# Kernel optimization log

Hardware: AMD Instinct MI355X
Metric: run time of the kernel (lower is better)

Reference implementation:

```python
import jax, jax.numpy as jnp
import numpy as np

NEG_INF = -jnp.inf


def _bilinear_resize(x, out_h, out_w):
    """Matches torch F.interpolate(mode='bilinear', align_corners=False, antialias=False).
    x: [N, C, H, W] -> [N, C, out_h, out_w]."""
    N, C, H, W = x.shape

    def idx(in_s, out_s):
        scale = in_s / out_s
        src = jnp.maximum((jnp.arange(out_s, dtype=jnp.float32) + 0.5) * scale - 0.5, 0.0)
        i0 = jnp.floor(src).astype(jnp.int32)
        i1 = jnp.minimum(i0 + 1, in_s - 1)
        w = src - i0.astype(jnp.float32)
        return i0, i1, w

    y0, y1, wy = idx(H, out_h)
    x0, x1, wx = idx(W, out_w)
    # blend rows
    top = x[:, :, y0, :] * (1.0 - wy)[None, None, :, None] + x[:, :, y1, :] * wy[None, None, :, None]
    # blend cols
    out = top[:, :, :, x0] * (1.0 - wx)[None, None, None, :] + top[:, :, :, x1] * wx[None, None, None, :]
    return out


def _maxpool2(x):
    return jax.lax.reduce_window(x, NEG_INF, jax.lax.max,
                                 (1, 1, 2, 2), (1, 1, 2, 2), 'VALID')


def _lrelu(x):
    return jnp.where(x >= 0, x, 0.2 * x)


def setup_inputs() -> dict:
    key = jax.random.key(0)
    ks = jax.random.split(key, 6)
    N, C, H, W = 4, 32, 256, 256
    KS2 = 9
    psf = jax.random.normal(ks[0], (N, C, H, W), dtype=jnp.float32)
    featuremap = jax.random.normal(ks[1], (N, C, H, W), dtype=jnp.float32)
    w1 = jax.random.normal(ks[2], (C * KS2, C), dtype=jnp.float32) * 0.05
    b1 = jnp.zeros((C * KS2,), dtype=jnp.float32)
    ws = jax.random.normal(ks[3], (C * KS2, C), dtype=jnp.float32) * 0.05
    bs = jnp.zeros((C * KS2,), dtype=jnp.float32)
    return {"psf": psf, "featuremap": featuremap, "w1": w1, "b1": b1, "ws": ws, "bs": bs}


def reference(psf, featuremap, w1, b1, ws, bs):
    N, C, H, W = featuremap.shape
    KS = 3
    # psf branch: 1/4 bilinear -> maxpool2 -> KPResBlock (1x1 convs) -> x8 bilinear
    p = _bilinear_resize(psf, H // 4, W // 4)
    p = _maxpool2(p)                       # [N, C, H/8, W/8]
    identity = jnp.einsum('nchw,oc->nohw', p, ws) + bs[None, :, None, None]
    y = _lrelu(jnp.einsum('nchw,oc->nohw', p, w1) + b1[None, :, None, None]) + identity
    filt = _bilinear_resize(y, H, W)       # [N, C*9, H, W]
    # FAC: per-pixel dynamic 3x3 filter, fused (no materialized unfold)
    wflt = filt.reshape(N, C, KS * KS, H, W)
    padded = jnp.pad(featuremap, ((0, 0), (0, 0), (1, 1), (1, 1)))
    out = jnp.zeros((N, C, H, W), dtype=featuremap.dtype)
    for dy in range(KS):
        for dx in range(KS):
            out = out + padded[:, :, dy:dy + H, dx:dx + W] * wflt[:, :, dy * KS + dx]
    return out
```

## Files before the change

### kernel.cpp

```cpp
#include <hip/hip_runtime.h>

#define N_ 4
#define C_ 32
#define H_ 256
#define W_ 256
#define O_ 288
#define PH 32
#define P_ELEMS (N_*C_*PH*PH)
#define Y_ELEMS (N_*O_*PH*PH)
#define OUT_ELEMS (N_*C_*H_*W_)

__global__ __launch_bounds__(256) void k_downsample(
    const float* __restrict__ psf, float* __restrict__ p) {
  int tid = blockIdx.x * blockDim.x + threadIdx.x;
  if (tid >= P_ELEMS) return;
  int tx = tid & 31;
  int ty = (tid >> 5) & 31;
  int nc = tid >> 10;
  const float* x = psf + (size_t)nc * (H_ * W_);
  float m = -1e30f;
#pragma unroll
  for (int a = 0; a < 2; a++) {
#pragma unroll
    for (int b = 0; b < 2; b++) {
      int r0 = 8 * ty + 4 * a + 1;
      int c0 = 8 * tx + 4 * b + 1;
      const float* row0 = x + r0 * W_ + c0;
      const float* row1 = row0 + W_;
      float avg = 0.25f * (row0[0] + row0[1] + row1[0] + row1[1]);
      m = fmaxf(m, avg);
    }
  }
  p[tid] = m;
}

__global__ __launch_bounds__(256) void k_conv1x1(
    const float* __restrict__ p, const float* __restrict__ w1,
    const float* __restrict__ b1, const float* __restrict__ ws,
    const float* __restrict__ bs, float* __restrict__ y) {
  int bid = blockIdx.x;
  int n = bid / O_;
  int o = bid - n * O_;
  const float4* p4 = (const float4*)(p + (size_t)n * (C_ * PH * PH));
  const float* w1o = w1 + o * C_;
  const float* wso = ws + o * C_;
  float bb1 = b1[o];
  float bbs = bs[o];
  int t = threadIdx.x;
  float a1x = bb1, a1y = bb1, a1z = bb1, a1w = bb1;
  float a2x = bbs, a2y = bbs, a2z = bbs, a2w = bbs;
#pragma unroll
  for (int c = 0; c < C_; c++) {
    float4 pv = p4[c * 256 + t];
    float u1 = w1o[c], u2 = wso[c];
    a1x = fmaf(pv.x, u1, a1x); a1y = fmaf(pv.y, u1, a1y);
    a1z = fmaf(pv.z, u1, a1z); a1w = fmaf(pv.w, u1, a1w);
    a2x = fmaf(pv.x, u2, a2x); a2y = fmaf(pv.y, u2, a2y);
    a2z = fmaf(pv.z, u2, a2z); a2w = fmaf(pv.w, u2, a2w);
  }
  float4 r;
  r.x = ((a1x >= 0.f) ? a1x : 0.2f * a1x) + a2x;
  r.y = ((a1y >= 0.f) ? a1y : 0.2f * a1y) + a2y;
  r.z = ((a1z >= 0.f) ? a1z : 0.2f * a1z) + a2z;
  r.w = ((a1w >= 0.f) ? a1w : 0.2f * a1w) + a2w;
  ((float4*)(y + (size_t)bid * (PH * PH)))[t] = r;
}

__global__ __launch_bounds__(256) void k_fac(
    const float* __restrict__ fm, const float* __restrict__ y,
    float* __restrict__ out) {
  int bid = blockIdx.x;
  int work = (bid >> 3) + (bid & 7) * 512;
  int g = (work << 8) + threadIdx.x;
  int m = g & 31;
  int h = (g >> 5) & 255;
  int c = (g >> 13) & 31;
  int n = g >> 18;

  float sh = fmaxf(0.125f * (float)h - 0.4375f, 0.f);
  int y0 = (int)sh;
  float wy = sh - (float)y0;
  int y1 = min(y0 + 1, 31);

  int cm1 = max(m - 1, 0);
  int cp1 = min(m + 1, 31);
  int ro0 = y0 * 32, ro1 = y1 * 32;

  const float* yb = y + ((size_t)(n * O_ + c * 9) << 10);
  const float* fb = fm + ((size_t)(n * C_ + c) << 16);

  float acc0 = 0.f, acc1 = 0.f, acc2 = 0.f, acc3 = 0.f;
  float acc4 = 0.f, acc5 = 0.f, acc6 = 0.f, acc7 = 0.f;

#pragma unroll
  for (int ky = 0; ky < 3; ky++) {
    int row = h + ky - 1;
    float fv[10];
    if (row >= 0 && row < 256) {
      const float* fr = fb + row * 256 + (m << 3);
      float4 q0 = *(const float4*)(fr);
      float4 q1 = *(const float4*)(fr + 4);
      fv[0] = (m > 0) ? fr[-1] : 0.f;
      fv[1] = q0.x; fv[2] = q0.y; fv[3] = q0.z; fv[4] = q0.w;
      fv[5] = q1.x; fv[6] = q1.y; fv[7] = q1.z; fv[8] = q1.w;
      fv[9] = (m < 31) ? fr[8] : 0.f;
    } else {
#pragma unroll
      for (int t = 0; t < 10; t++) fv[t] = 0.f;
    }
#pragma unroll
    for (int kx = 0; kx < 3; kx++) {
      const float* yp = yb + ((3 * ky + kx) << 10);
      float t0 = yp[ro0 + cm1], t1 = yp[ro0 + m], t2 = yp[ro0 + cp1];
      float u0 = yp[ro1 + cm1], u1 = yp[ro1 + m], u2 = yp[ro1 + cp1];
      float tb0 = fmaf(wy, u0 - t0, t0);
      float tb1 = fmaf(wy, u1 - t1, t1);
      float tb2 = fmaf(wy, u2 - t2, t2);
      float d0 = tb1 - tb0;
      float d1 = tb2 - tb1;
      float yv0 = fmaf(0.5625f, d0, tb0);
      float yv1 = fmaf(0.6875f, d0, tb0);
      float yv2 = fmaf(0.8125f, d0, tb0);
      float yv3 = fmaf(0.9375f, d0, tb0);
      float yv4 = fmaf(0.0625f, d1, tb1);
      float yv5 = fmaf(0.1875f, d1, tb1);
      float yv6 = fmaf(0.3125f, d1, tb1);
      float yv7 = fmaf(0.4375f, d1, tb1);
      acc0 = fmaf(fv[0 + kx], yv0, acc0);
      acc1 = fmaf(fv[1 + kx], yv1, acc1);
      acc2 = fmaf(fv[2 + kx], yv2, acc2);
      acc3 = fmaf(fv[3 + kx], yv3, acc3);
      acc4 = fmaf(fv[4 + kx], yv4, acc4);
      acc5 = fmaf(fv[5 + kx], yv5, acc5);
      acc6 = fmaf(fv[6 + kx], yv6, acc6);
      acc7 = fmaf(fv[7 + kx], yv7, acc7);
    }
  }
  float* ob = out + ((size_t)(((n * C_ + c) << 8) + h) << 8) + (m << 3);
  float4 r0 = {acc0, acc1, acc2, acc3};
  float4 r1 = {acc4, acc5, acc6, acc7};
  *(float4*)(ob) = r0;
  *(float4*)(ob + 4) = r1;
}

extern "C" void kernel_launch(void* const* d_in, const int* in_sizes, int n_in,
                              void* d_out, int out_size, void* d_ws,
                              size_t ws_size, hipStream_t stream) {
  const float* psf = (const float*)d_in[0];
  const float* fm = (const float*)d_in[1];
  const float* w1 = (const float*)d_in[2];
  const float* b1 = (const float*)d_in[3];
  const float* ws = (const float*)d_in[4];
  const float* bs = (const float*)d_in[5];
  float* out = (float*)d_out;

  float* p = (float*)d_ws;
  float* y = p + P_ELEMS;

  k_downsample<<<P_ELEMS / 256, 256, 0, stream>>>(psf, p);
  k_conv1x1<<<N_ * O_, 256, 0, stream>>>(p, w1, b1, ws, bs, y);
  k_fac<<<OUT_ELEMS / (8 * 256), 256, 0, stream>>>(fm, y, out);
}
```

Before: 131.8 us.

## Interleave 9 filter taps per position in y and use nontemporal output stores

The conv1x1 kernel now computes all 9 taps for one channel per thread and writes them contiguously with a stride of 12 floats per spatial position. The FAC kernel can then gather the 6 neighbouring positions with vector loads and precompute the row blend once for all taps, replacing 54 scattered scalar loads with 12 vector loads plus 6 scalars. Output stores become nontemporal so they bypass cache pollution. The y buffer grows by the padding factor, and the conv kernel now runs fewer blocks, each with more registers.

```diff
diff --git a/kernel.cpp b/kernel.cpp
--- a/kernel.cpp
+++ b/kernel.cpp
@@ -4,11 +4,12 @@
 #define C_ 32
 #define H_ 256
 #define W_ 256
-#define O_ 288
 #define PH 32
+#define KSTRIDE 12
 #define P_ELEMS (N_*C_*PH*PH)
-#define Y_ELEMS (N_*O_*PH*PH)
 #define OUT_ELEMS (N_*C_*H_*W_)
+
+typedef float v4f __attribute__((ext_vector_type(4)));
 
 __global__ __launch_bounds__(256) void k_downsample(
     const float* __restrict__ psf, float* __restrict__ p) {
@@ -39,31 +40,36 @@
     const float* __restrict__ b1, const float* __restrict__ ws,
     const float* __restrict__ bs, float* __restrict__ y) {
   int bid = blockIdx.x;
-  int n = bid / O_;
-  int o = bid - n * O_;
-  const float4* p4 = (const float4*)(p + (size_t)n * (C_ * PH * PH));
-  const float* w1o = w1 + o * C_;
-  const float* wso = ws + o * C_;
-  float bb1 = b1[o];
-  float bbs = bs[o];
-  int t = threadIdx.x;
-  float a1x = bb1, a1y = bb1, a1z = bb1, a1w = bb1;
-  float a2x = bbs, a2y = bbs, a2z = bbs, a2w = bbs;
+  int q = bid & 3;
+  int c = (bid >> 2) & 31;
+  int n = bid >> 7;
+  int hw = (q << 8) + threadIdx.x;
+  const float* pn = p + ((n * C_) << 10) + hw;
+  float a1[9], a2[9];
 #pragma unroll
-  for (int c = 0; c < C_; c++) {
-    float4 pv = p4[c * 256 + t];
-    float u1 = w1o[c], u2 = wso[c];
-    a1x = fmaf(pv.x, u1, a1x); a1y = fmaf(pv.y, u1, a1y);
-    a1z = fmaf(pv.z, u1, a1z); a1w = fmaf(pv.w, u1, a1w);
-    a2x = fmaf(pv.x, u2, a2x); a2y = fmaf(pv.y, u2, a2y);
-    a2z = fmaf(pv.z, u2, a2z); a2w = fmaf(pv.w, u2, a2w);
+  for (int k = 0; k < 9; k++) {
+    a1[k] = b1[c * 9 + k];
+    a2[k] = bs[c * 9 + k];
   }
-  float4 r;
-  r.x = ((a1x >= 0.f) ? a1x : 0.2f * a1x) + a2x;
-  r.y = ((a1y >= 0.f) ? a1y : 0.2f * a1y) + a2y;
-  r.z = ((a1z >= 0.f) ? a1z : 0.2f * a1z) + a2z;
-  r.w = ((a1w >= 0.f) ? a1w : 0.2f * a1w) + a2w;
-  ((float4*)(y + (size_t)bid * (PH * PH)))[t] = r;
+#pragma unroll
+  for (int c2 = 0; c2 < C_; c2++) {
+    float pv = pn[c2 << 10];
+#pragma unroll
+    for (int k = 0; k < 9; k++) {
+      a1[k] = fmaf(pv, w1[(c * 9 + k) * C_ + c2], a1[k]);
+      a2[k] = fmaf(pv, ws[(c * 9 + k) * C_ + c2], a2[k]);
+    }
+  }
+  float r[9];
+#pragma unroll
+  for (int k = 0; k < 9; k++)
+    r[k] = ((a1[k] >= 0.f) ? a1[k] : 0.2f * a1[k]) + a2[k];
+  float* yo = y + (size_t)(((n * C_ + c) << 10) + hw) * KSTRIDE;
+  v4f v0 = {r[0], r[1], r[2], r[3]};
+  v4f v1 = {r[4], r[5], r[6], r[7]};
+  *(v4f*)yo = v0;
+  *(v4f*)(yo + 4) = v1;
+  yo[8] = r[8];
 }
 
 __global__ __launch_bounds__(256) void k_fac(
@@ -81,14 +87,31 @@
   int y0 = (int)sh;
   float wy = sh - (float)y0;
   int y1 = min(y0 + 1, 31);
-
   int cm1 = max(m - 1, 0);
   int cp1 = min(m + 1, 31);
-  int ro0 = y0 * 32, ro1 = y1 * 32;
 
-  const float* yb = y + ((size_t)(n * O_ + c * 9) << 10);
+  const float* yb = y + (size_t)((n * C_ + c) << 10) * KSTRIDE;
+  int pos[6] = {(y0 << 5) + cm1, (y0 << 5) + m, (y0 << 5) + cp1,
+                (y1 << 5) + cm1, (y1 << 5) + m, (y1 << 5) + cp1};
+  float P[6][9];
+#pragma unroll
+  for (int i = 0; i < 6; i++) {
+    const float* qp = yb + pos[i] * KSTRIDE;
+    v4f A = *(const v4f*)qp;
+    v4f B = *(const v4f*)(qp + 4);
+    P[i][0] = A.x; P[i][1] = A.y; P[i][2] = A.z; P[i][3] = A.w;
+    P[i][4] = B.x; P[i][5] = B.y; P[i][6] = B.z; P[i][7] = B.w;
+    P[i][8] = qp[8];
+  }
+  float TB0[9], TB1[9], TB2[9];
+#pragma unroll
+  for (int k = 0; k < 9; k++) {
+    TB0[k] = fmaf(wy, P[3][k] - P[0][k], P[0][k]);
+    TB1[k] = fmaf(wy, P[4][k] - P[1][k], P[1][k]);
+    TB2[k] = fmaf(wy, P[5][k] - P[2][k], P[2][k]);
+  }
+
   const float* fb = fm + ((size_t)(n * C_ + c) << 16);
-
   float acc0 = 0.f, acc1 = 0.f, acc2 = 0.f, acc3 = 0.f;
   float acc4 = 0.f, acc5 = 0.f, acc6 = 0.f, acc7 = 0.f;
 
@@ -97,9 +120,9 @@
     int row = h + ky - 1;
     float fv[10];
     if (row >= 0 && row < 256) {
-      const float* fr = fb + row * 256 + (m << 3);
-      float4 q0 = *(const float4*)(fr);
-      float4 q1 = *(const float4*)(fr + 4);
+      const float* fr = fb + (row << 8) + (m << 3);
+      v4f q0 = *(const v4f*)(fr);
+      v4f q1 = *(const v4f*)(fr + 4);
       fv[0] = (m > 0) ? fr[-1] : 0.f;
       fv[1] = q0.x; fv[2] = q0.y; fv[3] = q0.z; fv[4] = q0.w;
       fv[5] = q1.x; fv[6] = q1.y; fv[7] = q1.z; fv[8] = q1.w;
@@ -110,37 +133,24 @@
     }
 #pragma unroll
     for (int kx = 0; kx < 3; kx++) {
-      const float* yp = yb + ((3 * ky + kx) << 10);
-      float t0 = yp[ro0 + cm1], t1 = yp[ro0 + m], t2 = yp[ro0 + cp1];
-      float u0 = yp[ro1 + cm1], u1 = yp[ro1 + m], u2 = yp[ro1 + cp1];
-      float tb0 = fmaf(wy, u0 - t0, t0);
-      float tb1 = fmaf(wy, u1 - t1, t1);
-      float tb2 = fmaf(wy, u2 - t2, t2);
-      float d0 = tb1 - tb0;
-      float d1 = tb2 - tb1;
-      float yv0 = fmaf(0.5625f, d0, tb0);
-      float yv1 = fmaf(0.6875f, d0, tb0);
-      float yv2 = fmaf(0.8125f, d0, tb0);
-      float yv3 = fmaf(0.9375f, d0, tb0);
-      float yv4 = fmaf(0.0625f, d1, tb1);
-      float yv5 = fmaf(0.1875f, d1, tb1);
-      float yv6 = fmaf(0.3125f, d1, tb1);
-      float yv7 = fmaf(0.4375f, d1, tb1);
-      acc0 = fmaf(fv[0 + kx], yv0, acc0);
-      acc1 = fmaf(fv[1 + kx], yv1, acc1);
-      acc2 = fmaf(fv[2 + kx], yv2, acc2);
-      acc3 = fmaf(fv[3 + kx], yv3, acc3);
-      acc4 = fmaf(fv[4 + kx], yv4, acc4);
-      acc5 = fmaf(fv[5 + kx], yv5, acc5);
-      acc6 = fmaf(fv[6 + kx], yv6, acc6);
-      acc7 = fmaf(fv[7 + kx], yv7, acc7);
+      int k = 3 * ky + kx;
+      float d0 = TB1[k] - TB0[k];
+      float d1 = TB2[k] - TB1[k];
+      acc0 = fmaf(fv[0 + kx], fmaf(0.5625f, d0, TB0[k]), acc0);
+      acc1 = fmaf(fv[1 + kx], fmaf(0.6875f, d0, TB0[k]), acc1);
+      acc2 = fmaf(fv[2 + kx], fmaf(0.8125f, d0, TB0[k]), acc2);
+      acc3 = fmaf(fv[3 + kx], fmaf(0.9375f, d0, TB0[k]), acc3);
+      acc4 = fmaf(fv[4 + kx], fmaf(0.0625f, d1, TB1[k]), acc4);
+      acc5 = fmaf(fv[5 + kx], fmaf(0.1875f, d1, TB1[k]), acc5);
+      acc6 = fmaf(fv[6 + kx], fmaf(0.3125f, d1, TB1[k]), acc6);
+      acc7 = fmaf(fv[7 + kx], fmaf(0.4375f, d1, TB1[k]), acc7);
     }
   }
   float* ob = out + ((size_t)(((n * C_ + c) << 8) + h) << 8) + (m << 3);
-  float4 r0 = {acc0, acc1, acc2, acc3};
-  float4 r1 = {acc4, acc5, acc6, acc7};
-  *(float4*)(ob) = r0;
-  *(float4*)(ob + 4) = r1;
+  v4f r0 = {acc0, acc1, acc2, acc3};
+  v4f r1 = {acc4, acc5, acc6, acc7};
+  __builtin_nontemporal_store(r0, (v4f*)ob);
+  __builtin_nontemporal_store(r1, (v4f*)(ob + 4));
 }
 
 extern "C" void kernel_launch(void* const* d_in, const int* in_sizes, int n_in,
@@ -158,6 +168,6 @@
   float* y = p + P_ELEMS;
 
   k_downsample<<<P_ELEMS / 256, 256, 0, stream>>>(psf, p);
-  k_conv1x1<<<N_ * O_, 256, 0, stream>>>(p, w1, b1, ws, bs, y);
+  k_conv1x1<<<N_ * C_ * 4, 256, 0, stream>>>(p, w1, b1, ws, bs, y);
   k_fac<<<OUT_ELEMS / (8 * 256), 256, 0, stream>>>(fm, y, out);
 }
```

New measurement: 137.2 us. +4.1%, slower.
